# Optimization experiments

Hardware: AMD Instinct MI355X
Metric: run time of the kernel (lower is better)

## Reference

```python
import jax, jax.numpy as jnp
import numpy as np

B, N, L, C, K, NL, FF = 8, 2048, 2048, 256, 16, 2, 4
RADIUS = 0.12


def setup_inputs() -> dict:
    key = jax.random.key(0)
    ks = jax.random.split(key, 18)
    s = 0.02
    return {
        "q_xyz": jax.random.uniform(ks[0], (B, N, 3), dtype=jnp.float32),
        "q_feat": jax.random.normal(ks[1], (B, N, C), dtype=jnp.float32),
        "kv_xyz": jax.random.uniform(ks[2], (B, L, 3), dtype=jnp.float32),
        "kv_feat": jax.random.normal(ks[3], (B, L, C), dtype=jnp.float32),
        # PointTransformerConv linears (bias=False in PyG)
        "W_src": jax.random.normal(ks[4], (NL, C, C), dtype=jnp.float32) * s,
        "W_dst": jax.random.normal(ks[5], (NL, C, C), dtype=jnp.float32) * s,
        "W_lin": jax.random.normal(ks[6], (NL, C, C), dtype=jnp.float32) * s,
        # attn_nn = Linear(C,C)+ReLU (MLP plain_last=False)
        "W_attn": jax.random.normal(ks[7], (NL, C, C), dtype=jnp.float32) * s,
        "b_attn": jnp.zeros((NL, C), dtype=jnp.float32),
        # FFN
        "W1": jax.random.normal(ks[8], (NL, C, C * FF), dtype=jnp.float32) * s,
        "b1": jnp.zeros((NL, C * FF), dtype=jnp.float32),
        "W2": jax.random.normal(ks[9], (NL, C * FF, C), dtype=jnp.float32) * s,
        "b2": jnp.zeros((NL, C), dtype=jnp.float32),
        # LayerNorms
        "ln1_g": jnp.ones((NL, C), dtype=jnp.float32),
        "ln1_b": jnp.zeros((NL, C), dtype=jnp.float32),
        "ln2_g": jnp.ones((NL, C), dtype=jnp.float32),
        "ln2_b": jnp.zeros((NL, C), dtype=jnp.float32),
    }


def _ln(x, g, b, eps=1e-5):
    mu = x.mean(-1, keepdims=True)
    var = ((x - mu) ** 2).mean(-1, keepdims=True)
    return (x - mu) * jax.lax.rsqrt(var + eps) * g + b


def reference(q_xyz, q_feat, kv_xyz, kv_feat, W_src, W_dst, W_lin, W_attn,
              b_attn, W1, b1, W2, b2, ln1_g, ln1_b, ln2_g, ln2_b):
    # radius ball query: up to K nearest kv points within RADIUS of each query
    d2 = jnp.sum((q_xyz[:, :, None, :] - kv_xyz[:, None, :, :]) ** 2, axis=-1)  # [B,N,L]
    neg, idx = jax.lax.top_k(-d2, K)            # idx: [B,N,K] into L
    valid = (-neg) <= RADIUS * RADIUS           # [B,N,K] in-ball mask
    vmask = valid[..., None].astype(q_feat.dtype)

    gather = jax.vmap(lambda a, i: a[i])        # [B,L,C],[B,N,K] -> [B,N,K,C]
    out = q_feat
    for i in range(NL):
        a_src = kv_feat @ W_src[i]              # [B,L,C]
        a_dst = out @ W_dst[i]                  # [B,N,C]
        v = kv_feat @ W_lin[i]                  # [B,L,C]
        a_src_g = gather(a_src, idx)            # [B,N,K,C]
        v_g = gather(v, idx)                    # [B,N,K,C]
        # attn_nn(lin_dst(x_i) - lin_src(x_j) + delta), delta=0 (ZeroPos)
        alpha = jax.nn.relu(
            jnp.einsum('bnkc,cd->bnkd', a_dst[:, :, None, :] - a_src_g, W_attn[i]) + b_attn[i])
        logits = jnp.where(valid[..., None], alpha, -1e9)
        attn = jax.nn.softmax(logits, axis=2) * vmask   # per-channel softmax over neighbors
        conv = jnp.sum(attn * v_g, axis=2)              # [B,N,C]
        out = _ln(out + conv, ln1_g[i], ln1_b[i])
        h = jax.nn.gelu(out @ W1[i] + b1[i], approximate=False)
        out = _ln(out + h @ W2[i] + b2[i], ln2_g[i], ln2_b[i])
    return out
```

## Files before the change

kernel.cpp:

```cpp
#include <hip/hip_runtime.h>
#include <math.h>

#define BB 8
#define NN 2048
#define LL 2048
#define CC 256
#define KK 16
#define NL 2
#define FF 4

typedef __attribute__((ext_vector_type(8))) short short8v;
typedef __attribute__((ext_vector_type(4))) float f32x4;

__device__ __forceinline__ short f2b(float f) {
    unsigned u = __float_as_uint(f);
    u += 0x7FFFu + ((u >> 16) & 1u);
    return (short)(u >> 16);
}
__device__ __forceinline__ float b2f(short s) {
    return __uint_as_float(((unsigned)(unsigned short)s) << 16);
}
__device__ __forceinline__ float blo(unsigned u) {
    return __uint_as_float(u << 16);
}
__device__ __forceinline__ float bhi(unsigned u) {
    return __uint_as_float(u & 0xffff0000u);
}

__device__ __forceinline__ void g2l16(const void* g, void* l) {
    __builtin_amdgcn_global_load_lds(
        (const __attribute__((address_space(1))) void*)g,
        (__attribute__((address_space(3))) void*)l, 16, 0, 0);
}

__global__ __launch_bounds__(256) void init_k(const float* __restrict__ src,
                                              float* __restrict__ dst,
                                              short* __restrict__ dstb) {
    size_t i = ((size_t)blockIdx.x * 256 + threadIdx.x) * 4;
    float4 v = *reinterpret_cast<const float4*>(src + i);
    *reinterpret_cast<float4*>(dst + i) = v;
    short o[4] = {f2b(v.x), f2b(v.y), f2b(v.z), f2b(v.w)};
    *reinterpret_cast<int2*>(dstb + i) = *reinterpret_cast<int2*>(o);
}

__global__ __launch_bounds__(256) void f2b_k(const float* __restrict__ in,
                                             short* __restrict__ out) {
    size_t i = ((size_t)blockIdx.x * 256 + threadIdx.x) * 4;
    float4 v = *reinterpret_cast<const float4*>(in + i);
    short o[4] = {f2b(v.x), f2b(v.y), f2b(v.z), f2b(v.w)};
    *reinterpret_cast<int2*>(out + i) = *reinterpret_cast<int2*>(o);
}

__global__ __launch_bounds__(256) void tconvB_k(const float* __restrict__ W0,
                                                short* __restrict__ Wt0,
                                                int K, int N,
                                                size_t sin, size_t sout) {
    const float* W = W0 + (size_t)blockIdx.z * sin;
    short* Wt = Wt0 + (size_t)blockIdx.z * sout;
    __shared__ float tile[32][33];
    const int n0 = blockIdx.x * 32, k0 = blockIdx.y * 32;
    const int tx = threadIdx.x & 31, ty = threadIdx.x >> 5;
#pragma unroll
    for (int r = 0; r < 32; r += 8)
        tile[ty + r][tx] = W[(size_t)(k0 + ty + r) * N + n0 + tx];
    __syncthreads();
#pragma unroll
    for (int r = 0; r < 32; r += 8)
        Wt[(size_t)(n0 + ty + r) * K + k0 + tx] = f2b(tile[tx][ty + r]);
}

#define QPB 32
#define CAP 48
__global__ __launch_bounds__(256) void knn_k(const float* __restrict__ qxyz,
                                             const float* __restrict__ kvxyz,
                                             int* __restrict__ idx,
                                             float* __restrict__ valid) {
    __shared__ float4 sxyz[LL];
    __shared__ unsigned long long cpk[QPB][CAP + 1];
    __shared__ int ccnt[QPB];

    const int t   = threadIdx.x;
    const int q   = t >> 3;
    const int sub = t & 7;
    const int b   = blockIdx.x >> 6;
    const int n   = ((blockIdx.x & 63) << 5) + q;

    const float* kb = kvxyz + (size_t)b * LL * 3;
    for (int p = t; p < LL; p += 256)
        sxyz[p] = make_float4(kb[3 * p], kb[3 * p + 1], kb[3 * p + 2], 0.f);
    if (t < QPB) ccnt[t] = 0;
    __syncthreads();

    const size_t qo = (size_t)(b * NN + n) * 3;
    const float qx = qxyz[qo], qy = qxyz[qo + 1], qz = qxyz[qo + 2];
    const float rad2 = (float)(0.12 * 0.12);

    for (int j = sub; j < LL; j += 32) {
        float4 p0 = sxyz[j];
        float4 p1 = sxyz[j + 8];
        float4 p2 = sxyz[j + 16];
        float4 p3 = sxyz[j + 24];
        float x0 = qx - p0.x, y0 = qy - p0.y, z0 = qz - p0.z;
        float x1 = qx - p1.x, y1 = qy - p1.y, z1 = qz - p1.z;
        float x2 = qx - p2.x, y2 = qy - p2.y, z2 = qz - p2.z;
        float x3 = qx - p3.x, y3 = qy - p3.y, z3 = qz - p3.z;
        float d0 = fmaf(x0, x0, fmaf(y0, y0, z0 * z0));
        float d1 = fmaf(x1, x1, fmaf(y1, y1, z1 * z1));
        float d2 = fmaf(x2, x2, fmaf(y2, y2, z2 * z2));
        float d3 = fmaf(x3, x3, fmaf(y3, y3, z3 * z3));
        if (fminf(fminf(d0, d1), fminf(d2, d3)) <= rad2) {
            if (d0 <= rad2) {
                int s = atomicAdd(&ccnt[q], 1);
                if (s < CAP) cpk[q][s] = ((unsigned long long)__float_as_uint(d0) << 32) | (unsigned)(j);
            }
            if (d1 <= rad2) {
                int s = atomicAdd(&ccnt[q], 1);
                if (s < CAP) cpk[q][s] = ((unsigned long long)__float_as_uint(d1) << 32) | (unsigned)(j + 8);
            }
            if (d2 <= rad2) {
                int s = atomicAdd(&ccnt[q], 1);
                if (s < CAP) cpk[q][s] = ((unsigned long long)__float_as_uint(d2) << 32) | (unsigned)(j + 16);
            }
            if (d3 <= rad2) {
                int s = atomicAdd(&ccnt[q], 1);
                if (s < CAP) cpk[q][s] = ((unsigned long long)__float_as_uint(d3) << 32) | (unsigned)(j + 24);
            }
        }
    }
    __syncthreads();

    int c = ccnt[q]; if (c > CAP) c = CAP;
    const size_t o = (size_t)(b * NN + n) * KK;
#pragma unroll 1
    for (int j = sub; j < c; j += 8) {
        const unsigned long long v = cpk[q][j];
        int rank = 0;
#pragma unroll 1
        for (int i = 0; i < c; ++i) rank += (cpk[q][i] < v) ? 1 : 0;
        if (rank < KK) {
            idx[o + rank]   = (int)(v & 0xffffffffu);
            valid[o + rank] = 1.0f;
        }
    }
#pragma unroll
    for (int k = sub; k < KK; k += 8)
        if (k >= c) { idx[o + k] = 0; valid[o + k] = 0.0f; }
}

template <int ACT, int OBF>
__device__ __forceinline__ void mm_body(short* As, short* Bs,
                                        const short* __restrict__ A,
                                        const short* __restrict__ Bt,
                                        const float* __restrict__ bias,
                                        void* __restrict__ Cout,
                                        int N, int Kd, int bx, int by) {
    const int t = threadIdx.x;
    const int lane = t & 63;
    const int wv = t >> 6;
    const int wr = wv >> 1, wc = wv & 1;
    const int lrow = lane & 15;
    const int kc = lane >> 4;
    const int row0 = by * 128;
    const int col0 = bx * 128;

    f32x4 acc[4][4];
#pragma unroll
    for (int m = 0; m < 4; ++m)
#pragma unroll
        for (int n = 0; n < 4; ++n) acc[m][n] = f32x4{0.f, 0.f, 0.f, 0.f};

    const int r0 = t >> 2, cch = t & 3;
    const int scch = cch ^ ((r0 >> 1) & 3);

    for (int k0 = 0; k0 < Kd; k0 += 32) {
        __syncthreads();
        g2l16(A  + (size_t)(row0 + r0) * Kd + k0 + scch * 8,       As + t * 8);
        g2l16(A  + (size_t)(row0 + r0 + 64) * Kd + k0 + scch * 8,  As + 2048 + t * 8);
        g2l16(Bt + (size_t)(col0 + r0) * Kd + k0 + scch * 8,       Bs + t * 8);
        g2l16(Bt + (size_t)(col0 + r0 + 64) * Kd + k0 + scch * 8,  Bs + 2048 + t * 8);
        __syncthreads();
        short8v af[4], bf[4];
#pragma unroll
        for (int m = 0; m < 4; ++m) {
            const int ar = wr * 64 + m * 16 + lrow;
            af[m] = *(const short8v*)(As + ar * 32 + ((kc ^ ((ar >> 1) & 3)) * 8));
        }
#pragma unroll
        for (int n = 0; n < 4; ++n) {
            const int br = wc * 64 + n * 16 + lrow;
            bf[n] = *(const short8v*)(Bs + br * 32 + ((kc ^ ((br >> 1) & 3)) * 8));
        }
#pragma unroll
        for (int m = 0; m < 4; ++m)
#pragma unroll
            for (int n = 0; n < 4; ++n)
                acc[m][n] = __builtin_amdgcn_mfma_f32_16x16x32_bf16(
                    af[m], bf[n], acc[m][n], 0, 0, 0);
    }

    float bcol[4];
#pragma unroll
    for (int n = 0; n < 4; ++n)
        bcol[n] = bias ? bias[col0 + wc * 64 + n * 16 + lrow] : 0.f;

#pragma unroll
    for (int m = 0; m < 4; ++m) {
#pragma unroll
        for (int n = 0; n < 4; ++n) {
            const int col = col0 + wc * 64 + n * 16 + lrow;
#pragma unroll
            for (int r = 0; r < 4; ++r) {
                const int row = row0 + wr * 64 + m * 16 + kc * 4 + r;
                float v = acc[m][n][r] + bcol[n];
                if (ACT == 1) v = 0.5f * v * (1.0f + erff(v * 0.70710678118654752f));
                if (OBF) ((short*)Cout)[(size_t)row * N + col] = f2b(v);
                else     ((float*)Cout)[(size_t)row * N + col] = v;
            }
        }
    }
}

template <int ACT, int OBF>
__global__ __launch_bounds__(256) void mm_k(const short* __restrict__ A,
                                            const short* __restrict__ Bt,
                                            const float* __restrict__ bias,
                                            void* __restrict__ Cout,
                                            int M, int N, int Kd) {
    __shared__ __align__(16) short As[128 * 32];
    __shared__ __align__(16) short Bs[128 * 32];
    mm_body<ACT, OBF>(As, Bs, A, Bt, bias, Cout, N, Kd, blockIdx.x, blockIdx.y);
    (void)M;
}

__global__ __launch_bounds__(256) void mmpair_k(
    const short* A0, const short* Bt0, void* C0, int N0,
    const short* A1, const short* Bt1, void* C1, int N1, int Kd) {
    __shared__ __align__(16) short As[128 * 32];
    __shared__ __align__(16) short Bs[128 * 32];
    const int nb0 = N0 >> 7;
    if ((int)blockIdx.x < nb0)
        mm_body<0, 1>(As, Bs, A0, Bt0, nullptr, C0, N0, Kd, blockIdx.x, blockIdx.y);
    else
        mm_body<0, 1>(As, Bs, A1, Bt1, nullptr, C1, N1, Kd, blockIdx.x - nb0, blockIdx.y);
}

__global__ __launch_bounds__(256) void wcomb_k(const short* __restrict__ WatT,
                                               const short* __restrict__ Wdst16,
                                               const short* __restrict__ Wsrc16,
                                               short* __restrict__ WcdT,
                                               short* __restrict__ Wsv) {
    __shared__ __align__(16) short As[128 * 32];
    __shared__ __align__(16) short Bs[128 * 32];
    const int z = blockIdx.z, i = z >> 1, sel = z & 1;
    const short* A = WatT + (size_t)i * CC * CC;
    const short* B = (sel ? Wsrc16 : Wdst16) + (size_t)i * CC * CC;
    short* C = sel ? (Wsv + (size_t)i * 2 * CC * CC) : (WcdT + (size_t)i * CC * CC);
    mm_body<0, 1>(As, Bs, A, B, nullptr, C, CC, CC, blockIdx.x, blockIdx.y);
}

#define AQB 4
__global__ __launch_bounds__(256) void attn_ln_k(
    const short* __restrict__ dw, const short* __restrict__ swv,
    const int* __restrict__ idx, const float* __restrict__ valid,
    const float* __restrict__ bat,
    const float* __restrict__ ln_g, const float* __restrict__ ln_b,
    float* __restrict__ out, short* __restrict__ outb) {
    __shared__ int   sidx[AQB * KK];
    __shared__ float sval[AQB * KK];
    __shared__ __align__(16) float sconv[AQB][CC];
    const int t = threadIdx.x;
    const int b   = blockIdx.x & 7;
    const int blk = blockIdx.x >> 3;
    const int bn0 = b * NN + blk * AQB;
    const size_t boff = (size_t)b * LL;

    if (t < AQB * KK) {
        sidx[t] = idx[(size_t)bn0 * KK + t];
        sval[t] = valid[(size_t)bn0 * KK + t];
    }
    __syncthreads();

    const int cp = (t & 127) * 2;
    const int qh = t >> 7;
    const float bias0 = bat[cp], bias1 = bat[cp + 1];
    const unsigned* swvu = (const unsigned*)swv;

#pragma unroll
    for (int qq = 0; qq < 2; ++qq) {
        const int q = qh * 2 + qq;
        const int bn = bn0 + q;
        const unsigned du = *(const unsigned*)(dw + (size_t)bn * CC + cp);
        const float d0 = blo(du) + bias0;
        const float d1 = bhi(du) + bias1;
        float s0 = 0.f, s1 = 0.f, n0 = 0.f, n1 = 0.f;
#pragma unroll
        for (int k = 0; k < KK; ++k) {
            const int j = sidx[q * KK + k];
            const float vv = sval[q * KK + k];
            const unsigned* rp = swvu + (boff + j) * CC;
            const unsigned su = rp[cp >> 1];
            const unsigned vu = rp[128 + (cp >> 1)];
            const float e0 = vv * __expf(fmaxf(d0 - blo(su), 0.f));
            const float e1 = vv * __expf(fmaxf(d1 - bhi(su), 0.f));
            s0 += e0; s1 += e1;
            n0 = fmaf(e0, blo(vu), n0);
            n1 = fmaf(e1, bhi(vu), n1);
        }
        sconv[q][cp]     = (s0 > 0.f) ? n0 / s0 : 0.f;
        sconv[q][cp + 1] = (s1 > 0.f) ? n1 / s1 : 0.f;
    }
    __syncthreads();

    const int lane = t & 63, w = t >> 6;
    float4 gg = *reinterpret_cast<const float4*>(&ln_g[lane * 4]);
    float4 bb = *reinterpret_cast<const float4*>(&ln_b[lane * 4]);
    {
        const int q = w;
        const size_t base = (size_t)(bn0 + q) * CC + lane * 4;
        float4 x = *reinterpret_cast<const float4*>(&out[base]);
        float4 d = *reinterpret_cast<const float4*>(&sconv[q][lane * 4]);
        float v0 = x.x + d.x, v1 = x.y + d.y, v2 = x.z + d.z, v3 = x.w + d.w;
        float s = v0 + v1 + v2 + v3;
#pragma unroll
        for (int o = 32; o > 0; o >>= 1) s += __shfl_xor(s, o);
        const float mu = s * (1.0f / 256.0f);
        const float t0 = v0 - mu, t1 = v1 - mu, t2 = v2 - mu, t3 = v3 - mu;
        float qv = t0 * t0 + t1 * t1 + t2 * t2 + t3 * t3;
#pragma unroll
        for (int o = 32; o > 0; o >>= 1) qv += __shfl_xor(qv, o);
        const float rstd = rsqrtf(qv * (1.0f / 256.0f) + 1e-5f);
        float4 y;
        y.x = t0 * rstd * gg.x + bb.x;
        y.y = t1 * rstd * gg.y + bb.y;
        y.z = t2 * rstd * gg.z + bb.z;
        y.w = t3 * rstd * gg.w + bb.w;
        *reinterpret_cast<float4*>(&out[base]) = y;
        short o4[4] = {f2b(y.x), f2b(y.y), f2b(y.z), f2b(y.w)};
        *reinterpret_cast<int2*>(outb + base) = *reinterpret_cast<int2*>(o4);
    }
}

__global__ __launch_bounds__(256) void add_ln_k(float* __restrict__ out,
                                                const float* __restrict__ del,
                                                const float* __restrict__ g,
                                                const float* __restrict__ bt,
                                                short* __restrict__ ob) {
    const int row  = blockIdx.x * 4 + (threadIdx.x >> 6);
    const int lane = threadIdx.x & 63;
    const size_t base = (size_t)row * CC + lane * 4;
    float4 x = *reinterpret_cast<const float4*>(&out[base]);
    float4 d = *reinterpret_cast<const float4*>(&del[base]);
    float v0 = x.x + d.x, v1 = x.y + d.y, v2 = x.z + d.z, v3 = x.w + d.w;

    float s = v0 + v1 + v2 + v3;
#pragma unroll
    for (int o = 32; o > 0; o >>= 1) s += __shfl_xor(s, o);
    const float mu = s * (1.0f / 256.0f);
    const float t0 = v0 - mu, t1 = v1 - mu, t2 = v2 - mu, t3 = v3 - mu;
    float q = t0 * t0 + t1 * t1 + t2 * t2 + t3 * t3;
#pragma unroll
    for (int o = 32; o > 0; o >>= 1) q += __shfl_xor(q, o);
    const float rstd = rsqrtf(q * (1.0f / 256.0f) + 1e-5f);

    float4 gg = *reinterpret_cast<const float4*>(&g[lane * 4]);
    float4 bb = *reinterpret_cast<const float4*>(&bt[lane * 4]);
    float4 y;
    y.x = t0 * rstd * gg.x + bb.x;
    y.y = t1 * rstd * gg.y + bb.y;
    y.z = t2 * rstd * gg.z + bb.z;
    y.w = t3 * rstd * gg.w + bb.w;
    *reinterpret_cast<float4*>(&out[base]) = y;
    short o4[4] = {f2b(y.x), f2b(y.y), f2b(y.z), f2b(y.w)};
    *reinterpret_cast<int2*>(ob + base) = *reinterpret_cast<int2*>(o4);
}

extern "C" void kernel_launch(void* const* d_in, const int* in_sizes, int n_in,
                              void* d_out, int out_size, void* d_ws, size_t ws_size,
                              hipStream_t stream) {
    const float* q_xyz   = (const float*)d_in[0];
    const float* q_feat  = (const float*)d_in[1];
    const float* kv_xyz  = (const float*)d_in[2];
    const float* kv_feat = (const float*)d_in[3];
    const float* W_src   = (const float*)d_in[4];
    const float* W_dst   = (const float*)d_in[5];
    const float* W_lin   = (const float*)d_in[6];
    const float* W_attn  = (const float*)d_in[7];
    const float* b_attn  = (const float*)d_in[8];
    const float* W1      = (const float*)d_in[9];
    const float* b1      = (const float*)d_in[10];
    const float* W2      = (const float*)d_in[11];
    const float* b2      = (const float*)d_in[12];
    const float* ln1_g   = (const float*)d_in[13];
    const float* ln1_b   = (const float*)d_in[14];
    const float* ln2_g   = (const float*)d_in[15];
    const float* ln2_b   = (const float*)d_in[16];

    float* out = (float*)d_out;
    char* wsb = (char*)d_ws;
    const size_t MB = (size_t)1 << 20;
    int*   idxb   = (int*)(wsb);
    float* validb = (float*)(wsb + 1 * MB);
    short* kvf16  = (short*)(wsb + 2 * MB);
    short* outb16 = (short*)(wsb + 10 * MB);
    short* dw16   = (short*)(wsb + 18 * MB);
    short* swv16  = (short*)(wsb + 26 * MB);
    short* h16    = (short*)(wsb + 42 * MB);
    float* convb  = (float*)(wsb + 74 * MB);
    short* WatT   = (short*)(wsb + 90 * MB);
    short* Wdst16 = (short*)(wsb + 90 * MB + 256 * 1024);
    short* Wsrc16 = (short*)(wsb + 90 * MB + 512 * 1024);
    short* WcdT   = (short*)(wsb + 90 * MB + 768 * 1024);
    short* Wsv    = (short*)(wsb + 91 * MB);
    short* W1T    = (short*)(wsb + 92 * MB);
    short* W2T    = (short*)(wsb + 93 * MB);

    const int M = BB * NN;

    init_k<<<M * CC / (256 * 4), 256, 0, stream>>>(q_feat, out, outb16);
    f2b_k<<<M * CC / (256 * 4), 256, 0, stream>>>(kv_feat, kvf16);
    f2b_k<<<NL * CC * CC / (256 * 4), 256, 0, stream>>>(W_dst, Wdst16);
    f2b_k<<<NL * CC * CC / (256 * 4), 256, 0, stream>>>(W_src, Wsrc16);
    knn_k<<<BB * (NN / QPB), 256, 0, stream>>>(q_xyz, kv_xyz, idxb, validb);

    tconvB_k<<<dim3(8, 8, NL), 256, 0, stream>>>(W_attn, WatT, CC, CC,
                                                 (size_t)CC * CC, (size_t)CC * CC);
    tconvB_k<<<dim3(8, 8, NL), 256, 0, stream>>>(W_lin, Wsv + CC * CC, CC, CC,
                                                 (size_t)CC * CC, (size_t)2 * CC * CC);
    tconvB_k<<<dim3(32, 8, NL), 256, 0, stream>>>(W1, W1T, CC, CC * FF,
                                                  (size_t)CC * CC * FF, (size_t)CC * CC * FF);
    tconvB_k<<<dim3(8, 32, NL), 256, 0, stream>>>(W2, W2T, CC * FF, CC,
                                                  (size_t)CC * CC * FF, (size_t)CC * CC * FF);
    wcomb_k<<<dim3(2, 2, 2 * NL), 256, 0, stream>>>(WatT, Wdst16, Wsrc16, WcdT, Wsv);

    for (int i = 0; i < NL; ++i) {
        const size_t oF = (size_t)i * CC * CC * FF;
        const size_t oC = (size_t)i * CC * CC;
        const float* bat = b_attn + (size_t)i * CC;
        const float* b1p = b1 + (size_t)i * CC * FF;
        const float* b2p = b2 + (size_t)i * CC;

        mmpair_k<<<dim3(6, 128), 256, 0, stream>>>(
            outb16, WcdT + oC, dw16, CC,
            kvf16, Wsv + (size_t)i * 2 * CC * CC, swv16, 2 * CC, CC);

        attn_ln_k<<<M / AQB, 256, 0, stream>>>(dw16, swv16, idxb, validb, bat,
                                               ln1_g + (size_t)i * CC, ln1_b + (size_t)i * CC,
                                               out, outb16);

        mm_k<1, 1><<<dim3(8, 128), 256, 0, stream>>>(outb16, W1T + oF, b1p, h16, M, CC * FF, CC);
        mm_k<0, 0><<<dim3(2, 128), 256, 0, stream>>>(h16, W2T + oF, b2p, convb, M, CC, CC * FF);
        add_ln_k<<<M / 4, 256, 0, stream>>>(out, convb,
                                            ln2_g + (size_t)i * CC, ln2_b + (size_t)i * CC, outb16);
    }
    (void)in_sizes; (void)n_in; (void)out_size; (void)ws_size;
}
```

Before: 283.8 us.

## Fuse W2 GEMM with residual LayerNorm and hoist kv projections out of layer loop

Adds a w2ln_k kernel that computes the FFN down-projection with 64-row by 256-column tiles, so each block holds full rows. It then applies bias, the residual add and LayerNorm in the epilogue, removing the fp32 convb round trip and the separate add_ln_k launch. The kv-side src/value projections for both layers are computed once before the loop as a single 1024-wide GEMM, and attention indexes the wider row with a per-layer offset. The fused kernel uses 64 fp32 accumulators per lane and fewer blocks (256), so occupancy and parallelism may drop, and its epilogue does strided scalar stores.

```diff
diff --git a/kernel.cpp b/kernel.cpp
--- a/kernel.cpp
+++ b/kernel.cpp
@@ -232,18 +232,6 @@
     (void)M;
 }
 
-__global__ __launch_bounds__(256) void mmpair_k(
-    const short* A0, const short* Bt0, void* C0, int N0,
-    const short* A1, const short* Bt1, void* C1, int N1, int Kd) {
-    __shared__ __align__(16) short As[128 * 32];
-    __shared__ __align__(16) short Bs[128 * 32];
-    const int nb0 = N0 >> 7;
-    if ((int)blockIdx.x < nb0)
-        mm_body<0, 1>(As, Bs, A0, Bt0, nullptr, C0, N0, Kd, blockIdx.x, blockIdx.y);
-    else
-        mm_body<0, 1>(As, Bs, A1, Bt1, nullptr, C1, N1, Kd, blockIdx.x - nb0, blockIdx.y);
-}
-
 __global__ __launch_bounds__(256) void wcomb_k(const short* __restrict__ WatT,
                                                const short* __restrict__ Wdst16,
                                                const short* __restrict__ Wsrc16,
@@ -256,6 +244,86 @@
     const short* B = (sel ? Wsrc16 : Wdst16) + (size_t)i * CC * CC;
     short* C = sel ? (Wsv + (size_t)i * 2 * CC * CC) : (WcdT + (size_t)i * CC * CC);
     mm_body<0, 1>(As, Bs, A, B, nullptr, C, CC, CC, blockIdx.x, blockIdx.y);
+}
+
+#define W2BM 64
+__global__ __launch_bounds__(256) void w2ln_k(
+    const short* __restrict__ A,
+    const short* __restrict__ Bt,
+    const float* __restrict__ bias,
+    const float* __restrict__ ln_g, const float* __restrict__ ln_b,
+    float* __restrict__ out, short* __restrict__ outb) {
+    __shared__ __align__(16) short As[W2BM * 32];
+    __shared__ __align__(16) short Bs[256 * 32];
+    const int t = threadIdx.x;
+    const int lane = t & 63;
+    const int wv = t >> 6;
+    const int lrow = lane & 15;
+    const int kc = lane >> 4;
+    const int row0 = blockIdx.x * W2BM;
+    const int Kd = CC * FF;
+
+    f32x4 acc[16];
+#pragma unroll
+    for (int n = 0; n < 16; ++n) acc[n] = f32x4{0.f, 0.f, 0.f, 0.f};
+
+    const int r0 = t >> 2, cch = t & 3;
+    const int scch = cch ^ ((r0 >> 1) & 3);
+
+    for (int k0 = 0; k0 < Kd; k0 += 32) {
+        __syncthreads();
+        g2l16(A  + (size_t)(row0 + r0) * Kd + k0 + scch * 8, As + t * 8);
+        g2l16(Bt + (size_t)(r0      ) * Kd + k0 + scch * 8, Bs + t * 8);
+        g2l16(Bt + (size_t)(r0 +  64) * Kd + k0 + scch * 8, Bs + 2048 + t * 8);
+        g2l16(Bt + (size_t)(r0 + 128) * Kd + k0 + scch * 8, Bs + 4096 + t * 8);
+        g2l16(Bt + (size_t)(r0 + 192) * Kd + k0 + scch * 8, Bs + 6144 + t * 8);
+        __syncthreads();
+        const int ar = wv * 16 + lrow;
+        short8v af = *(const short8v*)(As + ar * 32 + ((kc ^ ((ar >> 1) & 3)) * 8));
+#pragma unroll
+        for (int n = 0; n < 16; ++n) {
+            const int br = n * 16 + lrow;
+            short8v bf = *(const short8v*)(Bs + br * 32 + ((kc ^ ((br >> 1) & 3)) * 8));
+            acc[n] = __builtin_amdgcn_mfma_f32_16x16x32_bf16(af, bf, acc[n], 0, 0, 0);
+        }
+    }
+
+#pragma unroll
+    for (int n = 0; n < 16; ++n) {
+        const int col = n * 16 + lrow;
+        const float bc = bias[col];
+#pragma unroll
+        for (int r = 0; r < 4; ++r) {
+            const int row = row0 + wv * 16 + kc * 4 + r;
+            acc[n][r] += bc + out[(size_t)row * CC + col];
+        }
+    }
+#pragma unroll
+    for (int r = 0; r < 4; ++r) {
+        float s = 0.f;
+#pragma unroll
+        for (int n = 0; n < 16; ++n) s += acc[n][r];
+        s += __shfl_xor(s, 1); s += __shfl_xor(s, 2);
+        s += __shfl_xor(s, 4); s += __shfl_xor(s, 8);
+        const float mu = s * (1.0f / 256.0f);
+        float q = 0.f;
+#pragma unroll
+        for (int n = 0; n < 16; ++n) {
+            const float d = acc[n][r] - mu;
+            q = fmaf(d, d, q);
+        }
+        q += __shfl_xor(q, 1); q += __shfl_xor(q, 2);
+        q += __shfl_xor(q, 4); q += __shfl_xor(q, 8);
+        const float rstd = rsqrtf(q * (1.0f / 256.0f) + 1e-5f);
+        const int row = row0 + wv * 16 + kc * 4 + r;
+#pragma unroll
+        for (int n = 0; n < 16; ++n) {
+            const int col = n * 16 + lrow;
+            const float y = (acc[n][r] - mu) * rstd * ln_g[col] + ln_b[col];
+            out[(size_t)row * CC + col] = y;
+            outb[(size_t)row * CC + col] = f2b(y);
+        }
+    }
 }
 
 #define AQB 4
@@ -297,7 +365,7 @@
         for (int k = 0; k < KK; ++k) {
             const int j = sidx[q * KK + k];
             const float vv = sval[q * KK + k];
-            const unsigned* rp = swvu + (boff + j) * CC;
+            const unsigned* rp = swvu + (boff + j) * 512;
             const unsigned su = rp[cp >> 1];
             const unsigned vu = rp[128 + (cp >> 1)];
             const float e0 = vv * __expf(fmaxf(d0 - blo(su), 0.f));
@@ -338,40 +406,6 @@
         short o4[4] = {f2b(y.x), f2b(y.y), f2b(y.z), f2b(y.w)};
         *reinterpret_cast<int2*>(outb + base) = *reinterpret_cast<int2*>(o4);
     }
-}
-
-__global__ __launch_bounds__(256) void add_ln_k(float* __restrict__ out,
-                                                const float* __restrict__ del,
-                                                const float* __restrict__ g,
-                                                const float* __restrict__ bt,
-                                                short* __restrict__ ob) {
-    const int row  = blockIdx.x * 4 + (threadIdx.x >> 6);
-    const int lane = threadIdx.x & 63;
-    const size_t base = (size_t)row * CC + lane * 4;
-    float4 x = *reinterpret_cast<const float4*>(&out[base]);
-    float4 d = *reinterpret_cast<const float4*>(&del[base]);
-    float v0 = x.x + d.x, v1 = x.y + d.y, v2 = x.z + d.z, v3 = x.w + d.w;
-
-    float s = v0 + v1 + v2 + v3;
-#pragma unroll
-    for (int o = 32; o > 0; o >>= 1) s += __shfl_xor(s, o);
-    const float mu = s * (1.0f / 256.0f);
-    const float t0 = v0 - mu, t1 = v1 - mu, t2 = v2 - mu, t3 = v3 - mu;
-    float q = t0 * t0 + t1 * t1 + t2 * t2 + t3 * t3;
-#pragma unroll
-    for (int o = 32; o > 0; o >>= 1) q += __shfl_xor(q, o);
-    const float rstd = rsqrtf(q * (1.0f / 256.0f) + 1e-5f);
-
-    float4 gg = *reinterpret_cast<const float4*>(&g[lane * 4]);
-    float4 bb = *reinterpret_cast<const float4*>(&bt[lane * 4]);
-    float4 y;
-    y.x = t0 * rstd * gg.x + bb.x;
-    y.y = t1 * rstd * gg.y + bb.y;
-    y.z = t2 * rstd * gg.z + bb.z;
-    y.w = t3 * rstd * gg.w + bb.w;
-    *reinterpret_cast<float4*>(&out[base]) = y;
-    short o4[4] = {f2b(y.x), f2b(y.y), f2b(y.z), f2b(y.w)};
-    *reinterpret_cast<int2*>(ob + base) = *reinterpret_cast<int2*>(o4);
 }
 
 extern "C" void kernel_launch(void* const* d_in, const int* in_sizes, int n_in,
@@ -403,9 +437,8 @@
     short* kvf16  = (short*)(wsb + 2 * MB);
     short* outb16 = (short*)(wsb + 10 * MB);
     short* dw16   = (short*)(wsb + 18 * MB);
-    short* swv16  = (short*)(wsb + 26 * MB);
-    short* h16    = (short*)(wsb + 42 * MB);
-    float* convb  = (float*)(wsb + 74 * MB);
+    short* swv2   = (short*)(wsb + 26 * MB);
+    short* h16    = (short*)(wsb + 58 * MB);
     short* WatT   = (short*)(wsb + 90 * MB);
     short* Wdst16 = (short*)(wsb + 90 * MB + 256 * 1024);
     short* Wsrc16 = (short*)(wsb + 90 * MB + 512 * 1024);
@@ -432,6 +465,9 @@
                                                   (size_t)CC * CC * FF, (size_t)CC * CC * FF);
     wcomb_k<<<dim3(2, 2, 2 * NL), 256, 0, stream>>>(WatT, Wdst16, Wsrc16, WcdT, Wsv);
 
+    mm_k<0, 1><<<dim3(8, 128), 256, 0, stream>>>(kvf16, Wsv, nullptr, swv2,
+                                                 M, 4 * CC, CC);
+
     for (int i = 0; i < NL; ++i) {
         const size_t oF = (size_t)i * CC * CC * FF;
         const size_t oC = (size_t)i * CC * CC;
@@ -439,18 +475,17 @@
         const float* b1p = b1 + (size_t)i * CC * FF;
         const float* b2p = b2 + (size_t)i * CC;
 
-        mmpair_k<<<dim3(6, 128), 256, 0, stream>>>(
-            outb16, WcdT + oC, dw16, CC,
-            kvf16, Wsv + (size_t)i * 2 * CC * CC, swv16, 2 * CC, CC);
-
-        attn_ln_k<<<M / AQB, 256, 0, stream>>>(dw16, swv16, idxb, validb, bat,
+        mm_k<0, 1><<<dim3(2, 128), 256, 0, stream>>>(outb16, WcdT + oC, nullptr, dw16, M, CC, CC);
+
+        attn_ln_k<<<M / AQB, 256, 0, stream>>>(dw16, swv2 + (size_t)i * 512,
+                                               idxb, validb, bat,
                                                ln1_g + (size_t)i * CC, ln1_b + (size_t)i * CC,
                                                out, outb16);
 
         mm_k<1, 1><<<dim3(8, 128), 256, 0, stream>>>(outb16, W1T + oF, b1p, h16, M, CC * FF, CC);
-        mm_k<0, 0><<<dim3(2, 128), 256, 0, stream>>>(h16, W2T + oF, b2p, convb, M, CC, CC * FF);
-        add_ln_k<<<M / 4, 256, 0, stream>>>(out, convb,
-                                            ln2_g + (size_t)i * CC, ln2_b + (size_t)i * CC, outb16);
+        w2ln_k<<<M / W2BM, 256, 0, stream>>>(h16, W2T + oF, b2p,
+                                             ln2_g + (size_t)i * CC, ln2_b + (size_t)i * CC,
+                                             out, outb16);
     }
     (void)in_sizes; (void)n_in; (void)out_size; (void)ws_size;
 }
```

Result: no change. 284.5 us (+0.2%).
